# Kernel tuning notes

Measured on AMD Instinct MI355X. Metric: run time of the kernel, lower is better.

## Reference

```python
import jax, jax.numpy as jnp
import numpy as np

DIM = 128
HEADS = 8
WS = 4  # window_size = size/11 = 44/11
HID = DIM * 4  # ffn_expansion_factor=4


def layernorm_cl(x, w, b):
    # WithBias LayerNorm over channel dim; x: (b,c,h,w)
    x3 = x.transpose(0, 2, 3, 1)  # b,h,w,c
    mu = x3.mean(-1, keepdims=True)
    var = ((x3 - mu) ** 2).mean(-1, keepdims=True)
    y = (x3 - mu) / jnp.sqrt(var + 1e-5) * w + b
    return y.transpose(0, 3, 1, 2)


def win_part(t, ws):
    # (b,c,h,w) -> (b*nh*nw, ws*ws, c), matching torch view/permute/contiguous
    b, c, h, w = t.shape
    t = t.reshape(b, c, h // ws, ws, w // ws, ws)
    t = t.transpose(0, 2, 4, 3, 5, 1)
    return t.reshape(b * (h // ws) * (w // ws), ws * ws, c)


def conv1x1(x, w):
    # w: (Cout, Cin, 1, 1)
    return jnp.einsum('bchw,oc->bohw', x, w[:, :, 0, 0])


def dwconv3(x, w):
    # depthwise 3x3, padding 1; w: (C,1,3,3)
    return jax.lax.conv_general_dilated(
        x, w, window_strides=(1, 1), padding=[(1, 1), (1, 1)],
        dimension_numbers=('NCHW', 'OIHW', 'NCHW'),
        feature_group_count=x.shape[1])


def setup_inputs() -> dict:
    key = jax.random.key(0)
    ks = jax.random.split(key, 10)
    b, c, h, w = 4, DIM, 176, 176
    inp = {
        'x': jax.random.normal(ks[0], (b, c, h, w), jnp.float32),
        'mask': jax.random.uniform(ks[1], (b, 1, 44, 44), jnp.float32),
        'edge': jax.random.normal(ks[2], (b, c, 44, 44), jnp.float32),
        'ln1_w': jnp.ones((c,), jnp.float32),
        'ln1_b': jnp.zeros((c,), jnp.float32),
        'Wq': jax.random.normal(ks[3], (c, c), jnp.float32) * 0.02,
        'Wk': jax.random.normal(ks[4], (c, c), jnp.float32) * 0.02,
        'Wv': jax.random.normal(ks[5], (c, c), jnp.float32) * 0.02,
        'ln2_w': jnp.ones((c,), jnp.float32),
        'ln2_b': jnp.zeros((c,), jnp.float32),
        'w_in': jax.random.normal(ks[6], (2 * HID, c, 1, 1), jnp.float32) * 0.02,
        'w_dw': jax.random.normal(ks[7], (2 * HID, 1, 3, 3), jnp.float32) * 0.1,
        'w_out': jax.random.normal(ks[8], (c, HID, 1, 1), jnp.float32) * 0.02,
    }
    return inp


def _forward(x, mask, edge, ln1_w, ln1_b, Wq, Wk, Wv, ln2_w, ln2_b, w_in, w_dw, w_out):
    b, c, h, w = x.shape
    d = c // HEADS
    scale = d ** (-0.5)

    # --- attention branch ---
    xn = layernorm_cl(x, ln1_w, ln1_b)
    x0 = xn

    edge_r = jax.image.resize(edge, (b, c, h, w), method='bilinear')
    mask_r = jax.image.resize(mask, (b, mask.shape[1], h, w), method='bilinear')

    q = win_part(edge_r, WS) @ Wq.T                 # (Bw, N, c)
    x0w = win_part(x0 * mask_r, WS)
    k = x0w @ Wk.T
    v = x0w @ Wv.T

    Bw, N = q.shape[0], q.shape[1]
    q = q.reshape(Bw, N, HEADS, d)
    k = k.reshape(Bw, N, HEADS, d)
    v = v.reshape(Bw, N, HEADS, d)

    # NB: faithful to original einsum -- contracts over heads axis, giving
    # per-token d x d channel attention.
    dots = jnp.einsum('bnij,bnik->bnjk', q, k) * scale  # (Bw, N, d, d)
    attn = jax.nn.softmax(dots, axis=-1)
    out = jnp.einsum('bnjk,bnik->bnij', attn, v)        # (Bw, N, HEADS, d)
    out = out.reshape(Bw, N, c)

    # faithful (non-inverse) window merge: view -> permute -> view
    out = out.reshape(b, h // WS, w // WS, WS * WS * c)
    out = out.transpose(0, 3, 1, 2).reshape(b, c, h, w)

    x = x + out

    # --- GDFN feedforward ---
    y = layernorm_cl(x, ln2_w, ln2_b)
    y = conv1x1(y, w_in)
    y = dwconv3(y, w_dw)
    y1, y2 = jnp.split(y, 2, axis=1)
    y = jax.nn.gelu(y1, approximate=False) * y2
    y = conv1x1(y, w_out)
    return x + y


def reference(x, mask, edge, ln1_w, ln1_b, Wq, Wk, Wv, ln2_w, ln2_b, w_in, w_dw, w_out):
    return _forward(x, mask, edge, ln1_w, ln1_b, Wq, Wk, Wv, ln2_w, ln2_b, w_in, w_dw, w_out)
```

## Files before the change

kernel.cpp:

```cpp
#include <hip/hip_runtime.h>
#include <hip/hip_bf16.h>
#include <math.h>

typedef __hip_bfloat16 bf16;
typedef short bf16x8 __attribute__((ext_vector_type(8)));
typedef short bf16x4 __attribute__((ext_vector_type(4)));
typedef float floatx4 __attribute__((ext_vector_type(4)));

#define YX 30976
#define NPOS (4*YX)

__device__ __forceinline__ float ldin(const void* p, size_t i, int bf) {
  return bf ? __bfloat162float(((const bf16*)p)[i]) : ((const float*)p)[i];
}

__device__ __forceinline__ void unpack8(bf16x8 v, float* f) {
  const unsigned* u = (const unsigned*)&v;
#pragma unroll
  for (int i = 0; i < 4; ++i) {
    f[2 * i]     = __uint_as_float(u[i] << 16);
    f[2 * i + 1] = __uint_as_float(u[i] & 0xffff0000u);
  }
}

__device__ __forceinline__ void glds16(const void* g, void* l) {
  __builtin_amdgcn_global_load_lds(
      (const __attribute__((address_space(1))) unsigned int*)g,
      (__attribute__((address_space(3))) unsigned int*)l, 16, 0, 0);
}

__device__ __forceinline__ void tap44(int o, int& i0, int& i1, float& f) {
  int t = o >> 2, r = o & 3;
  int base = (r < 2) ? (t - 1) : t;
  f = (r == 0) ? 0.625f : (r == 1) ? 0.875f : (r == 2) ? 0.125f : 0.375f;
  i0 = base < 0 ? 0 : base;
  i1 = (base + 1 > 43) ? 43 : base + 1;
}

__global__ void k_sniff(const unsigned* __restrict__ ln1w, int* __restrict__ flag) {
  if (threadIdx.x == 0 && blockIdx.x == 0)
    *flag = (*ln1w == 0x3F800000u) ? 0 : 1;
}

__global__ void __launch_bounds__(256) k_castw(
    const void* __restrict__ src, bf16* __restrict__ dst, int n,
    const int* __restrict__ flag) {
  int i = blockIdx.x * 256 + threadIdx.x;
  if (i >= n) return;
  int bf = *flag;
  dst[i] = bf ? ((const bf16*)src)[i]
              : __float2bfloat16(((const float*)src)[i]);
}

__global__ void __launch_bounds__(256) k_castdw(
    const void* __restrict__ src, bf16* __restrict__ dst,
    const int* __restrict__ flag) {
  int i = blockIdx.x * 256 + threadIdx.x;
  if (i >= 9216) return;
  int bf = *flag;
  int ch = i & 511, tap = (i >> 9) % 9, g = i / (512 * 9);
  float v = ldin(src, (size_t)(g * 512 + ch) * 9 + tap, bf);
  dst[(g * 9 + tap) * 512 + ch] = __float2bfloat16(v);
}

__global__ void __launch_bounds__(256) k_prep(
    const void* __restrict__ xin, const void* __restrict__ mask,
    const void* __restrict__ edge, const void* __restrict__ ln1w,
    const void* __restrict__ ln1b, const int* __restrict__ flag,
    bf16* __restrict__ e_buf, bf16* __restrict__ xm_buf,
    bf16* __restrict__ x_pm) {
  __shared__ float sP[4][64], ssP[4][64];
  __shared__ float smu[64], srstd[64], smv[64];
  __shared__ float slw[128], slb[128];
  __shared__ __align__(16) bf16 tileE[128 * 68];
  int bf = *flag;
  int tid = threadIdx.x;
  int p0 = blockIdx.x * 64;
  int b = p0 / YX, yx0 = p0 % YX;
  if (tid < 128) { slw[tid] = ldin(ln1w, tid, bf); slb[tid] = ldin(ln1b, tid, bf); }
  int pp = tid & 63, cq = tid >> 6;

  float vals[32], s = 0.f, ss = 0.f;
  {
    size_t base = ((size_t)(b * 128 + cq * 32)) * YX + yx0 + pp;
#pragma unroll
    for (int j = 0; j < 32; ++j) {
      float v = ldin(xin, base + (size_t)j * YX, bf);
      vals[j] = v; s += v; ss += v * v;
    }
  }
  sP[cq][pp] = s; ssP[cq][pp] = ss;
  __syncthreads();

  if (tid < 64) {
    float st  = sP[0][tid] + sP[1][tid] + sP[2][tid] + sP[3][tid];
    float sst = ssP[0][tid] + ssP[1][tid] + ssP[2][tid] + ssP[3][tid];
    float mu = st * (1.f / 128.f);
    float var = sst * (1.f / 128.f) - mu * mu;
    smu[tid] = mu;
    srstd[tid] = rsqrtf(fmaxf(var, 0.f) + 1e-5f);
    int gyx = yx0 + tid, y = gyx / 176, x = gyx % 176;
    int y0, y1, x0, x1; float fy, fx;
    tap44(y, y0, y1, fy); tap44(x, x0, x1, fx);
    size_t mb = (size_t)b * 1936;
    float m00 = ldin(mask, mb + y0 * 44 + x0, bf);
    float m01 = ldin(mask, mb + y0 * 44 + x1, bf);
    float m10 = ldin(mask, mb + y1 * 44 + x0, bf);
    float m11 = ldin(mask, mb + y1 * 44 + x1, bf);
    smv[tid] = (m00 * (1.f - fx) + m01 * fx) * (1.f - fy) +
               (m10 * (1.f - fx) + m11 * fx) * fy;
  }
  __syncthreads();

  {
    float mu = smu[pp], rstd = srstd[pp], mv = smv[pp];
    size_t ob = (size_t)(p0 + pp) * 128 + cq * 32;
#pragma unroll
    for (int j8 = 0; j8 < 4; ++j8) {
      bf16x8 xr, xmr;
#pragma unroll
      for (int i = 0; i < 8; ++i) {
        int j = j8 * 8 + i;
        float v = vals[j];
        int c = cq * 32 + j;
        ((bf16*)&xr)[i]  = __float2bfloat16(v);
        ((bf16*)&xmr)[i] = __float2bfloat16(((v - mu) * rstd * slw[c] + slb[c]) * mv);
      }
      *(bf16x8*)(x_pm + ob + j8 * 8)   = xr;
      *(bf16x8*)(xm_buf + ob + j8 * 8) = xmr;
    }
  }

  {
    int c = tid & 127, half = tid >> 7;
    size_t ebase = (size_t)(b * 128 + c) * 1936;
    int px = half * 32, pxend = px + 32;
    while (px < pxend) {
      int gyx = yx0 + px;
      int y = gyx / 176, x = gyx % 176;
      int seg = pxend - px;
      int rem = 176 - x;
      if (rem < seg) seg = rem;
      int y0, y1; float fy; tap44(y, y0, y1, fy);
      float fy0 = 1.f - fy;
      size_t r0 = ebase + (size_t)y0 * 44, r1 = ebase + (size_t)y1 * 44;
      int t = x >> 2;
      int tm = (t - 1 < 0) ? 0 : t - 1;
      int tp = (t + 1 > 43) ? 43 : t + 1;
      float Rm = fy0 * ldin(edge, r0 + tm, bf) + fy * ldin(edge, r1 + tm, bf);
      float R0 = fy0 * ldin(edge, r0 + t,  bf) + fy * ldin(edge, r1 + t,  bf);
      float Rp = fy0 * ldin(edge, r0 + tp, bf) + fy * ldin(edge, r1 + tp, bf);
      for (int g = 0; g < seg; g += 4) {
        bf16x4 pk;
        ((bf16*)&pk)[0] = __float2bfloat16(0.375f * Rm + 0.625f * R0);
        ((bf16*)&pk)[1] = __float2bfloat16(0.125f * Rm + 0.875f * R0);
        ((bf16*)&pk)[2] = __float2bfloat16(0.875f * R0 + 0.125f * Rp);
        ((bf16*)&pk)[3] = __float2bfloat16(0.625f * R0 + 0.375f * Rp);
        *(bf16x4*)&tileE[c * 68 + px + g] = pk;
        ++t;
        Rm = R0; R0 = Rp;
        int tn = (t + 1 > 43) ? 43 : t + 1;
        Rp = fy0 * ldin(edge, r0 + tn, bf) + fy * ldin(edge, r1 + tn, bf);
      }
      px += seg;
    }
  }
  __syncthreads();

  {
    size_t ob = (size_t)(p0 + pp) * 128 + cq * 32;
#pragma unroll
    for (int j8 = 0; j8 < 4; ++j8) {
      bf16x8 ev;
#pragma unroll
      for (int i = 0; i < 8; ++i)
        ((bf16*)&ev)[i] = tileE[(cq * 32 + j8 * 8 + i) * 68 + pp];
      *(bf16x8*)(e_buf + ob + j8 * 8) = ev;
    }
  }
}

__device__ __forceinline__ void gemm16x128_to_lds(
    const bf16* __restrict__ A, const bf16* __restrict__ W,
    bf16* __restrict__ Sdst, int m0, int lane) {
  int row = lane & 15, quad = lane >> 4, kq = quad * 8;
  floatx4 acc[8] = {};
#pragma unroll
  for (int kk = 0; kk < 4; ++kk) {
    bf16x8 a = *(const bf16x8*)(A + (size_t)(m0 + row) * 128 + kk * 32 + kq);
#pragma unroll
    for (int nt = 0; nt < 8; ++nt) {
      bf16x8 w = *(const bf16x8*)(W + (size_t)(nt * 16 + row) * 128 + kk * 32 + kq);
      acc[nt] = __builtin_amdgcn_mfma_f32_16x16x32_bf16(a, w, acc[nt], 0, 0, 0);
    }
  }
#pragma unroll
  for (int nt = 0; nt < 8; ++nt)
#pragma unroll
    for (int r = 0; r < 4; ++r)
      Sdst[(quad * 4 + r) * 128 + nt * 16 + row] = __float2bfloat16(acc[nt][r]);
}

__global__ void __launch_bounds__(256) k_qkvattn(
    const bf16* __restrict__ E, const bf16* __restrict__ XM,
    const bf16* __restrict__ Wq, const bf16* __restrict__ Wk,
    const bf16* __restrict__ Wv, bf16* __restrict__ O) {
  __shared__ __align__(16) bf16 sq[64 * 128];
  __shared__ __align__(16) bf16 sk[64 * 128];
  __shared__ __align__(16) bf16 sv[64 * 128];
  int wave = threadIdx.x >> 6, lane = threadIdx.x & 63;
  int m0 = blockIdx.x * 64 + wave * 16;
  gemm16x128_to_lds(E,  Wq, sq + wave * 2048, m0, lane);
  gemm16x128_to_lds(XM, Wk, sk + wave * 2048, m0, lane);
  gemm16x128_to_lds(XM, Wv, sv + wave * 2048, m0, lane);
  __syncthreads();

  int j = threadIdx.x & 15;
#pragma unroll
  for (int rr = 0; rr < 4; ++rr) {
    int tt = rr * 16 + (threadIdx.x >> 4);
    const bf16* q = sq + tt * 128;
    const bf16* k = sk + tt * 128;
    const bf16* v = sv + tt * 128;
    float qj[8];
#pragma unroll
    for (int i = 0; i < 8; ++i) qj[i] = __bfloat162float(q[i * 16 + j]);
    float s[16], mx = -1e30f;
#pragma unroll
    for (int kk = 0; kk < 16; ++kk) {
      float a = 0.f;
#pragma unroll
      for (int i = 0; i < 8; ++i) a += qj[i] * __bfloat162float(k[i * 16 + kk]);
      a *= 0.25f;
      s[kk] = a; mx = fmaxf(mx, a);
    }
    float sum = 0.f;
#pragma unroll
    for (int kk = 0; kk < 16; ++kk) { s[kk] = expf(s[kk] - mx); sum += s[kk]; }
    float inv = 1.f / sum;
    bf16x8 ov;
#pragma unroll
    for (int i = 0; i < 8; ++i) {
      float o = 0.f;
#pragma unroll
      for (int kk = 0; kk < 16; ++kk) o += s[kk] * __bfloat162float(v[i * 16 + kk]);
      ((bf16*)&ov)[i] = __float2bfloat16(o * inv);
    }
    *(bf16x8*)(O + (size_t)(blockIdx.x * 64 + tt) * 128 + j * 8) = ov;
  }
}

__global__ void __launch_bounds__(256) k_gemm2(
    const bf16* __restrict__ A, const bf16* __restrict__ W1,
    const bf16* __restrict__ W2, bf16* __restrict__ C1,
    bf16* __restrict__ C2) {
  __shared__ __align__(16) bf16 smem[20480];
  int tid = threadIdx.x;
  int wave = tid >> 6, lane = tid & 63;
  int row = lane & 15, kq8 = (lane >> 4) * 8;
  int m0b = blockIdx.x * 64;

  int srow = lane >> 2, scol = (lane & 3) * 8;
  const bf16* gA = A + (size_t)(m0b + wave * 16 + srow) * 128 + scol;
  const bf16* Wsrc = (wave < 2) ? W1 : W2;
  const bf16* gB = Wsrc + (size_t)((wave & 1) * 64 + srow) * 128 + scol;
  bf16* lA = smem + wave * 512;
  bf16* lB = smem + 2048 + wave * 2048;

  floatx4 acc[4][4] = {};
  glds16(gA, lA);
#pragma unroll
  for (int c = 0; c < 4; ++c) glds16(gB + c * 16 * 128, lB + c * 512);
  __syncthreads();

  int cur = 0;
  for (int t = 0; t < 4; ++t) {
    int nxt = cur ^ 1;
    if (t < 3) {
      const bf16* ga = gA + (t + 1) * 32;
      const bf16* gb = gB + (t + 1) * 32;
      glds16(ga, lA + nxt * 10240);
#pragma unroll
      for (int c = 0; c < 4; ++c)
        glds16(gb + c * 16 * 128, lB + nxt * 10240 + c * 512);
    }
    const bf16* sA = smem + cur * 10240;
    const bf16* sB = sA + 2048;
    bf16x8 af[4], bfr[4];
#pragma unroll
    for (int m = 0; m < 4; ++m)
      af[m] = *(const bf16x8*)(sA + (m * 16 + row) * 32 + kq8);
#pragma unroll
    for (int n = 0; n < 4; ++n)
      bfr[n] = *(const bf16x8*)(sB + (wave * 64 + n * 16 + row) * 32 + kq8);
#pragma unroll
    for (int m = 0; m < 4; ++m)
#pragma unroll
      for (int n = 0; n < 4; ++n)
        acc[m][n] = __builtin_amdgcn_mfma_f32_16x16x32_bf16(bfr[n], af[m], acc[m][n], 0, 0, 0);
    __syncthreads();
    cur = nxt;
  }

  bf16* dst = (wave < 2) ? C1 : C2;
  int j = lane & 15, quad = lane >> 4;
#pragma unroll
  for (int m = 0; m < 4; ++m) {
    size_t pb = (size_t)(m0b + m * 16 + j) * 128 + (wave & 1) * 64 + quad * 4;
#pragma unroll
    for (int n = 0; n < 4; ++n) {
      bf16x4 o;
#pragma unroll
      for (int r = 0; r < 4; ++r) ((bf16*)&o)[r] = __float2bfloat16(acc[m][n][r]);
      *(bf16x4*)(dst + pb + n * 16) = o;
    }
  }
}

__global__ void __launch_bounds__(256) k_merge(
    const bf16* __restrict__ AO2, const bf16* __restrict__ x_pm,
    const void* __restrict__ ln2w, const void* __restrict__ ln2b,
    const int* __restrict__ flag, bf16* __restrict__ resid,
    bf16* __restrict__ yln) {
  __shared__ __align__(16) bf16 stile[64 * 128];
  __shared__ float sP[4][64], ssP[4][64];
  __shared__ float smu[64], srstd[64];
  __shared__ float slw[128], slb[128];
  int bf = *flag;
  int tid = threadIdx.x;
  int bi = blockIdx.x;
  int iw0 = bi % 11, ih = (bi / 11) % 44, b = bi / 484;
  if (tid < 128) { slw[tid] = ldin(ln2w, tid, bf); slb[tid] = ldin(ln2b, tid, bf); }

#pragma unroll
  for (int q = 0; q < 4; ++q) {
    int idx = q * 256 + tid;
    int m = idx & 15, sp = idx >> 4;
    int dy = sp >> 4, wj = (sp >> 2) & 3, dx = sp & 3;
    int ys = ih * 4 + dy, xs = iw0 * 16 + wj * 4 + dx;
    bf16x8 v = *(const bf16x8*)(AO2 + (size_t)((b * 176 + ys) * 176 + xs) * 128 + m * 8);
    int opx = m * 4 + wj, n = dy * 4 + dx;
    *(bf16x8*)&stile[opx * 128 + (n ^ (opx & 15)) * 8] = v;
  }
  __syncthreads();

  int opx = tid & 63, cq = tid >> 6;
  int t = opx >> 2, wj = opx & 3;
  size_t p = (size_t)b * YX + t * 1936 + ih * 44 + iw0 * 4 + wj;
  float vals[32], s = 0.f, ss = 0.f;
#pragma unroll
  for (int j = 0; j < 4; ++j) {
    int nchunk = cq * 4 + j;
    bf16x8 av = *(const bf16x8*)&stile[opx * 128 + (nchunk ^ (opx & 15)) * 8];
    bf16x8 xv = *(const bf16x8*)(x_pm + p * 128 + cq * 32 + j * 8);
    float af[8], xf[8];
    unpack8(av, af); unpack8(xv, xf);
#pragma unroll
    for (int i = 0; i < 8; ++i) {
      float v = af[i] + xf[i];
      vals[j * 8 + i] = v; s += v; ss += v * v;
    }
  }
  sP[cq][opx] = s; ssP[cq][opx] = ss;
  __syncthreads();
  if (tid < 64) {
    float st  = sP[0][tid] + sP[1][tid] + sP[2][tid] + sP[3][tid];
    float sst = ssP[0][tid] + ssP[1][tid] + ssP[2][tid] + ssP[3][tid];
    float mu = st * (1.f / 128.f);
    float var = sst * (1.f / 128.f) - mu * mu;
    smu[tid] = mu;
    srstd[tid] = rsqrtf(fmaxf(var, 0.f) + 1e-5f);
  }
  __syncthreads();

  {
    float mu = smu[opx], rstd = srstd[opx];
    size_t ob = p * 128 + cq * 32;
#pragma unroll
    for (int j8 = 0; j8 < 4; ++j8) {
      bf16x8 rv, yv;
#pragma unroll
      for (int i = 0; i < 8; ++i) {
        int j = j8 * 8 + i;
        float v = vals[j];
        int c = cq * 32 + j;
        ((bf16*)&rv)[i] = __float2bfloat16(v);
        ((bf16*)&yv)[i] = __float2bfloat16((v - mu) * rstd * slw[c] + slb[c]);
      }
      *(bf16x8*)(resid + ob + j8 * 8) = rv;
      *(bf16x8*)(yln + ob + j8 * 8)   = yv;
    }
  }
}

__global__ void __launch_bounds__(256) k_dwgelu(
    const bf16* __restrict__ H1, const bf16* __restrict__ H2,
    const bf16* __restrict__ Wt, int j0, bf16* __restrict__ G) {
  int tid = blockIdx.x * 256 + threadIdx.x;
  int pos = tid >> 4, c8 = (tid & 15) * 8;
  int b = pos / YX, yx = pos % YX, y = yx / 176, x = yx % 176;
  float d1[8] = {}, d2[8] = {};
#pragma unroll
  for (int dy = 0; dy < 3; ++dy) {
    int ny = y + dy - 1;
    if (ny < 0 || ny > 175) continue;
#pragma unroll
    for (int dx = 0; dx < 3; ++dx) {
      int nx = x + dx - 1;
      if (nx < 0 || nx > 175) continue;
      int tap = dy * 3 + dx;
      size_t off = (size_t)(b * YX + ny * 176 + nx) * 128 + c8;
      float h1[8], h2[8], w1[8], w2[8];
      unpack8(*(const bf16x8*)(H1 + off), h1);
      unpack8(*(const bf16x8*)(H2 + off), h2);
      unpack8(*(const bf16x8*)(Wt + tap * 512 + j0 + c8), w1);
      unpack8(*(const bf16x8*)(Wt + (9 + tap) * 512 + j0 + c8), w2);
#pragma unroll
      for (int i = 0; i < 8; ++i) {
        d1[i] += w1[i] * h1[i];
        d2[i] += w2[i] * h2[i];
      }
    }
  }
  bf16x8 outv;
#pragma unroll
  for (int i = 0; i < 8; ++i) {
    float gl = 0.5f * d1[i] * (1.f + erff(d1[i] * 0.70710678118f));
    ((bf16*)&outv)[i] = __float2bfloat16(gl * d2[i]);
  }
  *(bf16x8*)(G + (size_t)pos * 512 + j0 + c8) = outv;
}

__global__ void __launch_bounds__(256) k_gemm_final(
    const bf16* __restrict__ G, const bf16* __restrict__ W,
    const bf16* __restrict__ resid, void* __restrict__ out,
    const int* __restrict__ flag) {
  __shared__ __align__(16) bf16 smem[16384];
  int tid = threadIdx.x;
  int wave = tid >> 6, lane = tid & 63;
  int row = lane & 15, kq8 = (lane >> 4) * 8;
  int wr = wave >> 1, wc = wave & 1;
  int m0b = blockIdx.x * 128;

  int srow = lane >> 2, scol = (lane & 3) * 8;
  const bf16* gA = G + (size_t)(m0b + wave * 32 + srow) * 512 + scol;
  const bf16* gB = W + (size_t)(wave * 32 + srow) * 512 + scol;
  bf16* lA = smem + wave * 1024;
  bf16* lB = smem + 4096 + wave * 1024;

  floatx4 acc[4][4] = {};
  glds16(gA, lA);            glds16(gA + 16 * 512, lA + 512);
  glds16(gB, lB);            glds16(gB + 16 * 512, lB + 512);
  __syncthreads();

  int cur = 0;
  for (int t = 0; t < 16; ++t) {
    int nxt = cur ^ 1;
    if (t < 15) {
      const bf16* ga = gA + (t + 1) * 32;
      const bf16* gb = gB + (t + 1) * 32;
      glds16(ga, lA + nxt * 8192);            glds16(ga + 16 * 512, lA + nxt * 8192 + 512);
      glds16(gb, lB + nxt * 8192);            glds16(gb + 16 * 512, lB + nxt * 8192 + 512);
    }
    const bf16* sA = smem + cur * 8192;
    const bf16* sB = sA + 4096;
    bf16x8 af[4], bfr[4];
#pragma unroll
    for (int m = 0; m < 4; ++m)
      af[m] = *(const bf16x8*)(sA + (wr * 64 + m * 16 + row) * 32 + kq8);
#pragma unroll
    for (int n = 0; n < 4; ++n)
      bfr[n] = *(const bf16x8*)(sB + (wc * 64 + n * 16 + row) * 32 + kq8);
#pragma unroll
    for (int m = 0; m < 4; ++m)
#pragma unroll
      for (int n = 0; n < 4; ++n)
        acc[m][n] = __builtin_amdgcn_mfma_f32_16x16x32_bf16(af[m], bfr[n], acc[m][n], 0, 0, 0);
    __syncthreads();
    cur = nxt;
  }

  {
    const bf16* gR = resid + (size_t)(m0b + wave * 32 + (lane >> 4)) * 128 + (lane & 15) * 8;
    bf16* lR = smem + wave * 32 * 128;
#pragma unroll
    for (int c = 0; c < 8; ++c)
      glds16(gR + (size_t)c * 4 * 128, lR + c * 4 * 128);
  }
  __syncthreads();

  int bfo = *flag;
  int b = m0b / YX, yx0 = m0b % YX;
  int j = lane & 15, quad = lane >> 4;
#pragma unroll
  for (int n = 0; n < 4; ++n) {
    int ch = wc * 64 + n * 16 + j;
    const bf16* rsl = smem + ch;
    size_t cb = (size_t)(b * 128 + ch) * YX + yx0;
#pragma unroll
    for (int m = 0; m < 4; ++m) {
      int pos = wr * 64 + m * 16 + quad * 4;
      float v[4];
#pragma unroll
      for (int r = 0; r < 4; ++r)
        v[r] = acc[m][n][r] + __bfloat162float(rsl[(pos + r) * 128]);
      if (bfo) {
        bf16x4 o;
#pragma unroll
        for (int r = 0; r < 4; ++r) ((bf16*)&o)[r] = __float2bfloat16(v[r]);
        *(bf16x4*)((bf16*)out + cb + pos) = o;
      } else {
        floatx4 o;
#pragma unroll
        for (int r = 0; r < 4; ++r) o[r] = v[r];
        *(floatx4*)((float*)out + cb + pos) = o;
      }
    }
  }
}

extern "C" void kernel_launch(void* const* d_in, const int* in_sizes, int n_in,
                              void* d_out, int out_size, void* d_ws, size_t ws_size,
                              hipStream_t stream) {
  const void* x    = d_in[0];
  const void* mask = d_in[1];
  const void* edge = d_in[2];
  const void* ln1w = d_in[3];
  const void* ln1b = d_in[4];
  const void* Wq   = d_in[5];
  const void* Wk   = d_in[6];
  const void* Wv   = d_in[7];
  const void* ln2w = d_in[8];
  const void* ln2b = d_in[9];
  const void* w_in = d_in[10];
  const void* w_dw = d_in[11];
  const void* w_out= d_in[12];

  char* ws = (char*)d_ws;
  const size_t SEG  = 31719424;
  const size_t GSZ  = 126877696;
  bf16* G     = (bf16*)(ws);
  bf16* B0    = (bf16*)(ws);
  bf16* B1    = (bf16*)(ws + GSZ);
  bf16* H1    = (bf16*)(ws + GSZ + SEG);
  bf16* H2    = (bf16*)(ws + GSZ + 2 * SEG);
  bf16* resid = (bf16*)(ws + GSZ + 3 * SEG);
  char* wsw   = ws + GSZ + 4 * SEG;
  bf16* wq_b   = (bf16*)(wsw);
  bf16* wk_b   = (bf16*)(wsw + 32768);
  bf16* wv_b   = (bf16*)(wsw + 65536);
  bf16* win_b  = (bf16*)(wsw + 98304);
  bf16* wout_b = (bf16*)(wsw + 98304 + 262144);
  bf16* wdwt_b = (bf16*)(wsw + 98304 + 262144 + 131072);
  int* flag    = (int*)(wsw + 98304 + 262144 + 131072 + 32768);

  k_sniff<<<1, 64, 0, stream>>>((const unsigned*)ln1w, flag);
  k_castw<<<64, 256, 0, stream>>>(Wq, wq_b, 16384, flag);
  k_castw<<<64, 256, 0, stream>>>(Wk, wk_b, 16384, flag);
  k_castw<<<64, 256, 0, stream>>>(Wv, wv_b, 16384, flag);
  k_castw<<<512, 256, 0, stream>>>(w_in, win_b, 131072, flag);
  k_castw<<<256, 256, 0, stream>>>(w_out, wout_b, 65536, flag);
  k_castdw<<<36, 256, 0, stream>>>(w_dw, wdwt_b, flag);

  k_prep<<<NPOS / 64, 256, 0, stream>>>(x, mask, edge, ln1w, ln1b, flag,
                                        B0, B1, H1 );
  k_qkvattn<<<NPOS / 64, 256, 0, stream>>>(B0, B1, wq_b, wk_b, wv_b, B0);
  k_merge<<<4 * 44 * 11, 256, 0, stream>>>(B0, H1 , ln2w, ln2b, flag,
                                           resid, B1);
  for (int j0 = 0; j0 < 512; j0 += 128) {
    k_gemm2<<<NPOS / 64, 256, 0, stream>>>(B1, win_b + (size_t)j0 * 128,
                                           win_b + (size_t)(512 + j0) * 128, H1, H2);
    k_dwgelu<<<NPOS * 16 / 256, 256, 0, stream>>>(H1, H2, wdwt_b, j0, G);
  }
  k_gemm_final<<<NPOS / 128, 256, 0, stream>>>(G, wout_b, resid, d_out, flag);
}
```

Measured before the change: 709.9 us.

## Restructure QKV-attention kernel with LDS-staged double-buffered MFMA and swizzled layouts

Rewrites the fused QKV projection plus channel attention kernel to use 384 threads (6 waves, two per Q/K/V matrix). Activation and weight tiles are staged into LDS with async global-to-LDS loads and double buffering over K, instead of each wave reading weights straight from global memory. Q/K are stored transposed in LDS with an XOR swizzle and V as fp32, so the softmax stage can use vector LDS reads and fast exp. It adds LDS pressure (64KB) and more barriers in exchange for better reuse of weights and less bank conflict.

```diff
diff --git a/kernel.cpp b/kernel.cpp
--- a/kernel.cpp
+++ b/kernel.cpp
@@ -180,73 +180,144 @@
   }
 }
 
-__device__ __forceinline__ void gemm16x128_to_lds(
-    const bf16* __restrict__ A, const bf16* __restrict__ W,
-    bf16* __restrict__ Sdst, int m0, int lane) {
-  int row = lane & 15, quad = lane >> 4, kq = quad * 8;
-  floatx4 acc[8] = {};
-#pragma unroll
-  for (int kk = 0; kk < 4; ++kk) {
-    bf16x8 a = *(const bf16x8*)(A + (size_t)(m0 + row) * 128 + kk * 32 + kq);
-#pragma unroll
-    for (int nt = 0; nt < 8; ++nt) {
-      bf16x8 w = *(const bf16x8*)(W + (size_t)(nt * 16 + row) * 128 + kk * 32 + kq);
-      acc[nt] = __builtin_amdgcn_mfma_f32_16x16x32_bf16(a, w, acc[nt], 0, 0, 0);
-    }
-  }
-#pragma unroll
-  for (int nt = 0; nt < 8; ++nt)
-#pragma unroll
-    for (int r = 0; r < 4; ++r)
-      Sdst[(quad * 4 + r) * 128 + nt * 16 + row] = __float2bfloat16(acc[nt][r]);
-}
-
-__global__ void __launch_bounds__(256) k_qkvattn(
+__global__ void __launch_bounds__(384, 3) k_qkvattn(
     const bf16* __restrict__ E, const bf16* __restrict__ XM,
     const bf16* __restrict__ Wq, const bf16* __restrict__ Wk,
     const bf16* __restrict__ Wv, bf16* __restrict__ O) {
-  __shared__ __align__(16) bf16 sq[64 * 128];
-  __shared__ __align__(16) bf16 sk[64 * 128];
-  __shared__ __align__(16) bf16 sv[64 * 128];
-  int wave = threadIdx.x >> 6, lane = threadIdx.x & 63;
-  int m0 = blockIdx.x * 64 + wave * 16;
-  gemm16x128_to_lds(E,  Wq, sq + wave * 2048, m0, lane);
-  gemm16x128_to_lds(XM, Wk, sk + wave * 2048, m0, lane);
-  gemm16x128_to_lds(XM, Wv, sv + wave * 2048, m0, lane);
-  __syncthreads();
-
-  int j = threadIdx.x & 15;
-#pragma unroll
-  for (int rr = 0; rr < 4; ++rr) {
-    int tt = rr * 16 + (threadIdx.x >> 4);
-    const bf16* q = sq + tt * 128;
-    const bf16* k = sk + tt * 128;
-    const bf16* v = sv + tt * 128;
-    float qj[8];
-#pragma unroll
-    for (int i = 0; i < 8; ++i) qj[i] = __bfloat162float(q[i * 16 + j]);
-    float s[16], mx = -1e30f;
-#pragma unroll
-    for (int kk = 0; kk < 16; ++kk) {
-      float a = 0.f;
-#pragma unroll
-      for (int i = 0; i < 8; ++i) a += qj[i] * __bfloat162float(k[i * 16 + kk]);
-      a *= 0.25f;
-      s[kk] = a; mx = fmaxf(mx, a);
-    }
-    float sum = 0.f;
-#pragma unroll
-    for (int kk = 0; kk < 16; ++kk) { s[kk] = expf(s[kk] - mx); sum += s[kk]; }
-    float inv = 1.f / sum;
-    bf16x8 ov;
-#pragma unroll
-    for (int i = 0; i < 8; ++i) {
-      float o = 0.f;
-#pragma unroll
-      for (int kk = 0; kk < 16; ++kk) o += s[kk] * __bfloat162float(v[i * 16 + kk]);
-      ((bf16*)&ov)[i] = __float2bfloat16(o * inv);
-    }
-    *(bf16x8*)(O + (size_t)(blockIdx.x * 64 + tt) * 128 + j * 8) = ov;
+  __shared__ __align__(16) bf16 smem[32768];
+  int tid = threadIdx.x;
+  int wave = tid / 64, lane = tid & 63;
+  int mat = wave >> 1, h = wave & 1;
+  int l15 = lane & 15, quad = lane >> 4;
+  int m0b = blockIdx.x * 64;
+
+  const bf16* gA = (mat == 0) ? E : XM;
+  const bf16* gW = (mat == 0) ? Wq : (mat == 1) ? Wk : Wv;
+
+  floatx4 acc[4][4] = {};
+
+#define STAGE(bb, kt)                                                          \
+  {                                                                            \
+    _Pragma("unroll")                                                          \
+    for (int c = 0; c < 4; ++c)                                                \
+      glds16(gW + (size_t)(h * 64 + c * 16 + l15) * 128 + (kt) + quad * 8,     \
+             smem + (bb) + 4096 + mat * 4096 + (h * 4 + c) * 512);             \
+    if (mat == 0) {                                                            \
+      _Pragma("unroll")                                                        \
+      for (int g = 0; g < 2; ++g) {                                            \
+        int mm = h * 2 + g;                                                    \
+        glds16(gA + (size_t)(m0b + mm * 16 + l15) * 128 + (kt) + quad * 8,     \
+               smem + (bb) + mm * 512);                                        \
+      }                                                                        \
+    } else {                                                                   \
+      int mm = wave - 2;                                                       \
+      glds16(gA + (size_t)(m0b + mm * 16 + l15) * 128 + (kt) + quad * 8,       \
+             smem + (bb) + 2048 + mm * 512);                                   \
+    }                                                                          \
+  }
+
+  STAGE(0, 0);
+  __syncthreads();
+
+  int cur = 0;
+  for (int t = 0; t < 4; ++t) {
+    int nb = cur ^ 16384;
+    if (t < 3) STAGE(nb, (t + 1) * 32);
+    const bf16* sA = smem + cur + (mat ? 2048 : 0);
+    const bf16* sW = smem + cur + 4096 + mat * 4096;
+    bf16x8 af[4], bfr[4];
+#pragma unroll
+    for (int m = 0; m < 4; ++m)
+      af[m] = *(const bf16x8*)(sA + m * 512 + lane * 8);
+#pragma unroll
+    for (int n = 0; n < 4; ++n)
+      bfr[n] = *(const bf16x8*)(sW + (h * 4 + n) * 512 + lane * 8);
+#pragma unroll
+    for (int m = 0; m < 4; ++m)
+#pragma unroll
+      for (int n = 0; n < 4; ++n)
+        acc[m][n] = __builtin_amdgcn_mfma_f32_16x16x32_bf16(bfr[n], af[m], acc[m][n], 0, 0, 0);
+    __syncthreads();
+    cur = nb;
+  }
+#undef STAGE
+
+  if (mat < 2) {
+    bf16* sT = smem + mat * 8192;
+    int key = l15 & 7;
+#pragma unroll
+    for (int m = 0; m < 4; ++m) {
+      int tokl = m * 16 + l15;
+#pragma unroll
+      for (int r = 0; r < 4; ++r) {
+        int cidx = quad * 4 + r;
+        bf16x4 o;
+#pragma unroll
+        for (int n = 0; n < 4; ++n) ((bf16*)&o)[n] = __float2bfloat16(acc[m][n][r]);
+        *(bf16x4*)(sT + tokl * 128 + ((cidx ^ key) * 8) + h * 4) = o;
+      }
+    }
+  } else {
+    float* sVf = (float*)(smem + 16384);
+    int key = l15 & 7;
+#pragma unroll
+    for (int m = 0; m < 4; ++m) {
+      int tokl = m * 16 + l15;
+#pragma unroll
+      for (int n = 0; n < 4; ++n) {
+        int ch4 = h * 16 + n * 4 + quad;
+        floatx4 o;
+#pragma unroll
+        for (int r = 0; r < 4; ++r) o[r] = acc[m][n][r];
+        *(floatx4*)(sVf + tokl * 128 + ((ch4 ^ key) << 2)) = o;
+      }
+    }
+  }
+  __syncthreads();
+
+  const bf16* sQt = smem;
+  const bf16* sKt = smem + 8192;
+  const float* sVf = (const float*)(smem + 16384);
+  for (int round = 0; round < 3; ++round) {
+    int item = round * 384 + tid;
+    if (item < 1024) {
+      int tt = item >> 4, j = item & 15;
+      int key = tt & 7;
+      float qv[8];
+      {
+        bf16x8 q8 = *(const bf16x8*)(sQt + tt * 128 + ((j ^ key) * 8));
+        unpack8(q8, qv);
+      }
+      float s[16], mx = -1e30f;
+#pragma unroll
+      for (int kk = 0; kk < 16; ++kk) {
+        bf16x8 k8 = *(const bf16x8*)(sKt + tt * 128 + ((kk ^ key) * 8));
+        float kv[8]; unpack8(k8, kv);
+        float a = 0.f;
+#pragma unroll
+        for (int i = 0; i < 8; ++i) a += qv[i] * kv[i];
+        a *= 0.25f;
+        s[kk] = a; mx = fmaxf(mx, a);
+      }
+      float sum = 0.f;
+#pragma unroll
+      for (int kk = 0; kk < 16; ++kk) { s[kk] = __expf(s[kk] - mx); sum += s[kk]; }
+      float inv = 1.f / sum;
+      bf16x8 ov;
+#pragma unroll
+      for (int i = 0; i < 8; ++i) {
+        float o = 0.f;
+#pragma unroll
+        for (int c4 = 0; c4 < 4; ++c4) {
+          int ch4 = i * 4 + c4;
+          floatx4 v4 = *(const floatx4*)(sVf + tt * 128 + ((ch4 ^ key) << 2));
+#pragma unroll
+          for (int r = 0; r < 4; ++r) o += s[c4 * 4 + r] * v4[r];
+        }
+        ((bf16*)&ov)[i] = __float2bfloat16(o * inv);
+      }
+      *(bf16x8*)(O + (size_t)(m0b + tt) * 128 + j * 8) = ov;
+    }
   }
 }
 
@@ -564,7 +635,7 @@
 
   k_prep<<<NPOS / 64, 256, 0, stream>>>(x, mask, edge, ln1w, ln1b, flag,
                                         B0, B1, H1 );
-  k_qkvattn<<<NPOS / 64, 256, 0, stream>>>(B0, B1, wq_b, wk_b, wv_b, B0);
+  k_qkvattn<<<NPOS / 64, 384, 0, stream>>>(B0, B1, wq_b, wk_b, wv_b, B0);
   k_merge<<<4 * 44 * 11, 256, 0, stream>>>(B0, H1 , ln2w, ln2b, flag,
                                            resid, B1);
   for (int j0 = 0; j0 < 512; j0 += 128) {
```

New measurement: 668.8 us. 1.06x faster.
